# Kernel optimization log

Hardware: AMD Instinct MI355X
Metric: run time of the kernel (lower is better)

Reference implementation:

```python
import jax, jax.numpy as jnp
import numpy as np

N_NODES = 100000
N_EDGES = 3200000
N_PAIRS = 500000
D_IN = 256
D_HID = 256
D_OUT = 2


def setup_inputs() -> dict:
    key = jax.random.key(0)
    ks = jax.random.split(key, 9)
    s1 = 1.0 / np.sqrt(D_IN)
    s2 = 1.0 / np.sqrt(D_HID)
    s3 = 1.0 / np.sqrt(2 * D_HID)
    return {
        "x": jax.random.normal(ks[0], (N_NODES, D_IN), jnp.float32),
        "edge_index": jax.random.randint(ks[1], (2, N_EDGES), 0, N_NODES, jnp.int64 if jax.config.jax_enable_x64 else jnp.int32),
        "index": jax.random.randint(ks[2], (N_PAIRS, 2), 0, N_NODES, jnp.int64 if jax.config.jax_enable_x64 else jnp.int32),
        "W1": jax.random.normal(ks[3], (D_HID, D_IN), jnp.float32) * s1,
        "b1": jnp.zeros((D_HID,), jnp.float32),
        "W2": jax.random.normal(ks[4], (D_HID, D_HID), jnp.float32) * s2,
        "b2": jnp.zeros((D_HID,), jnp.float32),
        "W3": jax.random.normal(ks[5], (D_OUT, 2 * D_HID), jnp.float32) * s3,
        "b3": jnp.zeros((D_OUT,), jnp.float32),
    }


def _gin_conv(x, edge_index, W, b):
    # PyG GINConv (eps=0): nn((1+eps)*x + sum_{j in N(i)} x_j)
    src, dst = edge_index[0], edge_index[1]
    agg = jax.ops.segment_sum(x[src], dst, num_segments=x.shape[0])  # [N, d]
    return (x + agg) @ W.T + b


def reference(x, edge_index, index, W1, b1, W2, b2, W3, b3):
    h = jax.nn.relu(_gin_conv(x, edge_index, W1, b1))   # [N, D_HID]
    h = jax.nn.relu(_gin_conv(h, edge_index, W2, b2))   # [N, D_HID]
    pair = jnp.concatenate((h[index[:, 0]], h[index[:, 1]]), axis=-1)  # [P, 2*D_HID]
    logits = pair @ W3.T + b3                            # [P, D_OUT]
    return jax.nn.log_softmax(logits, axis=1)
```

## Files before the change

### kernel.cpp

```cpp
#include <hip/hip_runtime.h>
#include <hip/hip_bf16.h>

constexpr int N_NODES = 100000;
constexpr int N_EDGES = 3200000;
constexpr int N_PAIRS = 500000;
constexpr int D       = 256;

using frag_ab = __attribute__((ext_vector_type(8))) short;
using frag_cd = __attribute__((ext_vector_type(4))) float;
typedef unsigned short ushort8 __attribute__((ext_vector_type(8)));

static __device__ __forceinline__ float b2f(unsigned short u) {
  return __uint_as_float(((unsigned)u) << 16);
}
static __device__ __forceinline__ unsigned short f2bf(float f) {
  unsigned u = __float_as_uint(f);
  unsigned r = (u + 0x7fff + ((u >> 16) & 1)) >> 16;
  return (unsigned short)r;
}

__global__ void zero_ints(int* __restrict__ p, int n) {
  int i = blockIdx.x * blockDim.x + threadIdx.x;
  if (i < n) p[i] = 0;
}

__global__ void copy_ints(const int* __restrict__ in, int* __restrict__ out, int n) {
  int i = blockIdx.x * blockDim.x + threadIdx.x;
  if (i < n) out[i] = in[i];
}

__global__ void f32_to_bf16(const float4* __restrict__ in, ushort4* __restrict__ out, int n4) {
  int i = blockIdx.x * blockDim.x + threadIdx.x;
  int stride = gridDim.x * blockDim.x;
  for (; i < n4; i += stride) {
    const float4 v = in[i];
    ushort4 o;
    o.x = f2bf(v.x); o.y = f2bf(v.y); o.z = f2bf(v.z); o.w = f2bf(v.w);
    out[i] = o;
  }
}

__global__ void hist_kernel(const int* __restrict__ ei, int* __restrict__ counts) {
  int i = blockIdx.x * blockDim.x + threadIdx.x;
  if (i < N_EDGES) atomicAdd(&counts[ei[N_EDGES + i]], 1);
}

__global__ __launch_bounds__(1024) void scan_kernel(const int* __restrict__ counts,
                                                    int* __restrict__ cursor, int n) {
  __shared__ int wsum[16];
  __shared__ int carry;
  const int t = threadIdx.x, lane = t & 63, w = t >> 6;
  if (t == 0) carry = 0;
  __syncthreads();
  for (int base = 0; base < n; base += 1024) {
    int v = (base + t < n) ? counts[base + t] : 0;
    int s = v;
#pragma unroll
    for (int off = 1; off < 64; off <<= 1) {
      int u = __shfl_up(s, off, 64);
      if (lane >= off) s += u;
    }
    if (lane == 63) wsum[w] = s;
    __syncthreads();
    if (t < 16) {
      int ws = wsum[t];
#pragma unroll
      for (int off = 1; off < 16; off <<= 1) {
        int u = __shfl_up(ws, off, 64);
        if (lane >= off) ws += u;
      }
      wsum[t] = ws;
    }
    __syncthreads();
    const int wpre = (w == 0) ? 0 : wsum[w - 1];
    if (base + t < n) cursor[base + t] = carry + wpre + s - v;
    __syncthreads();
    if (t == 0) carry += wsum[15];
    __syncthreads();
  }
}

constexpr int FILL_SEG = 4096;
__global__ __launch_bounds__(256) void fill_kernel(const int* __restrict__ ei,
                                                   int* __restrict__ pos,
                                                   int* __restrict__ csr) {
  const int range = blockIdx.x & 7;
  const int seg   = blockIdx.x >> 3;
  const int base  = seg * FILL_SEG;
  const int lo = range * 12500, hi = lo + 12500;
#pragma unroll
  for (int j = 0; j < FILL_SEG / 256; ++j) {
    const int i = base + j * 256 + threadIdx.x;
    if (i < N_EDGES) {
      const int dst = ei[N_EDGES + i];
      if (dst >= lo && dst < hi) {
        const int p = atomicAdd(&pos[dst], 1);
        csr[p] = ei[i];
      }
    }
  }
}

__global__ __launch_bounds__(256) void gather_agg_bf16(const ushort* __restrict__ x,
                                                       const int* __restrict__ csr,
                                                       const int* __restrict__ cursor,
                                                       const int* __restrict__ counts,
                                                       ushort* __restrict__ out) {
  const int node = blockIdx.x * 4 + (threadIdx.x >> 6);
  const int lane = threadIdx.x & 63;
  const int half = lane >> 5;
  const int fl   = lane & 31;
  if (node >= N_NODES) return;
  const int beg = cursor[node];
  const int end = beg + counts[node];
  const size_t fo = (size_t)fl * 8;

  float acc[8];
#pragma unroll
  for (int j = 0; j < 8; ++j) acc[j] = 0.f;

  if (half == 0) {
    const ushort8 self = *reinterpret_cast<const ushort8*>(x + (size_t)node * D + fo);
#pragma unroll
    for (int j = 0; j < 8; ++j) acc[j] += b2f(self[j]);
  }

  int o = beg + half;
  for (; o + 6 < end; o += 8) {
    const int s0 = csr[o], s1 = csr[o + 2], s2 = csr[o + 4], s3 = csr[o + 6];
    const ushort8 v0 = *reinterpret_cast<const ushort8*>(x + (size_t)s0 * D + fo);
    const ushort8 v1 = *reinterpret_cast<const ushort8*>(x + (size_t)s1 * D + fo);
    const ushort8 v2 = *reinterpret_cast<const ushort8*>(x + (size_t)s2 * D + fo);
    const ushort8 v3 = *reinterpret_cast<const ushort8*>(x + (size_t)s3 * D + fo);
#pragma unroll
    for (int j = 0; j < 8; ++j)
      acc[j] += (b2f(v0[j]) + b2f(v1[j])) + (b2f(v2[j]) + b2f(v3[j]));
  }
  for (; o < end; o += 2) {
    const ushort8 v = *reinterpret_cast<const ushort8*>(x + (size_t)csr[o] * D + fo);
#pragma unroll
    for (int j = 0; j < 8; ++j) acc[j] += b2f(v[j]);
  }

#pragma unroll
  for (int j = 0; j < 8; ++j) acc[j] += __shfl_xor(acc[j], 32, 64);

  if (half == 0) {
    ushort8 ov;
#pragma unroll
    for (int j = 0; j < 8; ++j) ov[j] = f2bf(acc[j]);
    *reinterpret_cast<ushort8*>(out + (size_t)node * D + fo) = ov;
  }
}

__global__ __launch_bounds__(256) void gemm_mfma_bf16(const ushort* __restrict__ A,
                                                      const ushort* __restrict__ W,
                                                      const float* __restrict__ bias,
                                                      ushort* __restrict__ C,
                                                      int M) {
  __shared__ __align__(16) ushort As[64 * 256];
  __shared__ __align__(16) ushort Ws[64 * 256];

  const int t = threadIdx.x;
  const int w = t >> 6, l = t & 63;
  const int row0 = blockIdx.x * 64;
  const int col0 = blockIdx.y * 64;

  {
    const float4 zero4 = {0.f, 0.f, 0.f, 0.f};
#pragma unroll
    for (int i = 0; i < 8; ++i) {
      const int chunk = t + i * 256;
      const int r  = chunk >> 5;
      const int kb = (chunk & 31) << 4;
      const int swz = kb ^ ((r & 7) << 4);
      const int grow = row0 + r;
      float4 av = zero4;
      if (grow < M)
        av = *reinterpret_cast<const float4*>(
            reinterpret_cast<const char*>(A) + (size_t)grow * 512 + kb);
      *reinterpret_cast<float4*>(reinterpret_cast<char*>(As) + r * 512 + swz) = av;
      const float4 wv = *reinterpret_cast<const float4*>(
          reinterpret_cast<const char*>(W) + (size_t)(col0 + r) * 512 + kb);
      *reinterpret_cast<float4*>(reinterpret_cast<char*>(Ws) + r * 512 + swz) = wv;
    }
  }
  __syncthreads();

  const int g  = l >> 4;
  const int fr = l & 15;

  frag_cd acc[4];
#pragma unroll
  for (int c = 0; c < 4; ++c) {
    acc[c][0] = 0.f; acc[c][1] = 0.f; acc[c][2] = 0.f; acc[c][3] = 0.f;
  }

  const int arow = w * 16 + fr;
  const char* Asb = reinterpret_cast<const char*>(As);
  const char* Wsb = reinterpret_cast<const char*>(Ws);
#pragma unroll
  for (int ks = 0; ks < 8; ++ks) {
    const int kb = ks * 64 + g * 16;
    const frag_ab af = *reinterpret_cast<const frag_ab*>(
        Asb + arow * 512 + (kb ^ ((arow & 7) << 4)));
#pragma unroll
    for (int c = 0; c < 4; ++c) {
      const int wrow = c * 16 + fr;
      const frag_ab bf = *reinterpret_cast<const frag_ab*>(
          Wsb + wrow * 512 + (kb ^ ((wrow & 7) << 4)));
      acc[c] = __builtin_amdgcn_mfma_f32_16x16x32_bf16(af, bf, acc[c], 0, 0, 0);
    }
  }
  __syncthreads();

  ushort* Ct = As;
#pragma unroll
  for (int c = 0; c < 4; ++c) {
    const int col = c * 16 + fr;
    const float bv = bias[col0 + col];
#pragma unroll
    for (int r = 0; r < 4; ++r) {
      const int rl = w * 16 + g * 4 + r;
      Ct[rl * 64 + col] = f2bf(fmaxf(acc[c][r] + bv, 0.f));
    }
  }
  __syncthreads();
#pragma unroll
  for (int i = 0; i < 2; ++i) {
    const int chunk = t + i * 256;
    const int r  = chunk >> 3;
    const int cb = (chunk & 7) << 4;
    const int grow = row0 + r;
    if (grow < M)
      *reinterpret_cast<float4*>(reinterpret_cast<char*>(C) + (size_t)grow * 512 + col0 * 2 + cb) =
          *reinterpret_cast<const float4*>(reinterpret_cast<const char*>(Ct) + r * 128 + cb);
  }
}

__global__ __launch_bounds__(256) void proj_kernel(const ushort* __restrict__ h,
                                                   const float* __restrict__ W3,
                                                   float4* __restrict__ proj) {
  const int node = blockIdx.x * 4 + (threadIdx.x >> 6);
  const int lane = threadIdx.x & 63;
  if (node >= N_NODES) return;

  const ushort4 hv = *reinterpret_cast<const ushort4*>(h + (size_t)node * D + lane * 4);
  const float h0 = b2f(hv.x), h1 = b2f(hv.y), h2 = b2f(hv.z), h3 = b2f(hv.w);

  const float4 wa0 = *reinterpret_cast<const float4*>(W3 + lane * 4);
  const float4 wa1 = *reinterpret_cast<const float4*>(W3 + 512 + lane * 4);
  const float4 wb0 = *reinterpret_cast<const float4*>(W3 + 256 + lane * 4);
  const float4 wb1 = *reinterpret_cast<const float4*>(W3 + 768 + lane * 4);

  float a0 = h0 * wa0.x + h1 * wa0.y + h2 * wa0.z + h3 * wa0.w;
  float a1 = h0 * wa1.x + h1 * wa1.y + h2 * wa1.z + h3 * wa1.w;
  float b0 = h0 * wb0.x + h1 * wb0.y + h2 * wb0.z + h3 * wb0.w;
  float b1 = h0 * wb1.x + h1 * wb1.y + h2 * wb1.z + h3 * wb1.w;

#pragma unroll
  for (int off = 32; off > 0; off >>= 1) {
    a0 += __shfl_xor(a0, off, 64);
    a1 += __shfl_xor(a1, off, 64);
    b0 += __shfl_xor(b0, off, 64);
    b1 += __shfl_xor(b1, off, 64);
  }
  if (lane == 0) {
    float4 o; o.x = a0; o.y = a1; o.z = b0; o.w = b1;
    proj[node] = o;
  }
}

__global__ __launch_bounds__(256) void pair_lite(const float4* __restrict__ proj,
                                                 const int* __restrict__ idx,
                                                 const float* __restrict__ b3,
                                                 float* __restrict__ out) {
  const int p = blockIdx.x * blockDim.x + threadIdx.x;
  if (p >= N_PAIRS) return;
  const int2 ii = reinterpret_cast<const int2*>(idx)[p];
  const float4 pa = proj[ii.x];
  const float4 pb = proj[ii.y];
  float l0 = pa.x + pb.z + b3[0];
  float l1 = pa.y + pb.w + b3[1];
  const float m = fmaxf(l0, l1);
  const float lse = m + logf(expf(l0 - m) + expf(l1 - m));
  float2 o; o.x = l0 - lse; o.y = l1 - lse;
  reinterpret_cast<float2*>(out)[p] = o;
}

extern "C" void kernel_launch(void* const* d_in, const int* in_sizes, int n_in,
                              void* d_out, int out_size, void* d_ws, size_t ws_size,
                              hipStream_t stream) {
  const float* x   = (const float*)d_in[0];
  const int*   ei  = (const int*)d_in[1];
  const int*   idx = (const int*)d_in[2];
  const float* W1  = (const float*)d_in[3];
  const float* b1  = (const float*)d_in[4];
  const float* W2  = (const float*)d_in[5];
  const float* b2  = (const float*)d_in[6];
  const float* W3  = (const float*)d_in[7];
  const float* b3  = (const float*)d_in[8];
  float* out = (float*)d_out;

  char* ws = (char*)d_ws;
  ushort* xb    = (ushort*)(ws);
  ushort* aggb  = (ushort*)(ws + 51200000);
  ushort* hb    = (ushort*)(ws + 102400000);
  ushort* W1b   = (ushort*)(ws + 153600000);
  ushort* W2b   = (ushort*)(ws + 153731072);
  int* counts   = (int*)(ws + 153862144);
  int* cursor   = (int*)(ws + 154262144);
  int* pos      = (int*)(ws + 154662144);
  int* csr      = (int*)(ws + 155062144);
  float4* proj  = (float4*)(ws + 167862144);

  const dim3 blk(256);
  const size_t feat = (size_t)N_NODES * D;
  const dim3 zeroGrid((N_NODES + 255) / 256);
  const dim3 edgeGrid((N_EDGES + 255) / 256);
  const int  nseg = (N_EDGES + FILL_SEG - 1) / FILL_SEG;
  const dim3 fillGrid(8 * nseg);
  const dim3 nodeGrid((N_NODES + 3) / 4);
  const dim3 gemmGrid((N_NODES + 63) / 64, D / 64);
  const dim3 pairGrid((N_PAIRS + 255) / 256);

  f32_to_bf16<<<dim3(4096), blk, 0, stream>>>((const float4*)x, (ushort4*)xb, (int)(feat / 4));
  f32_to_bf16<<<dim3(64), blk, 0, stream>>>((const float4*)W1, (ushort4*)W1b, 65536 / 4);
  f32_to_bf16<<<dim3(64), blk, 0, stream>>>((const float4*)W2, (ushort4*)W2b, 65536 / 4);

  zero_ints<<<zeroGrid, blk, 0, stream>>>(counts, N_NODES);
  hist_kernel<<<edgeGrid, blk, 0, stream>>>(ei, counts);
  scan_kernel<<<1, 1024, 0, stream>>>(counts, cursor, N_NODES);
  copy_ints<<<zeroGrid, blk, 0, stream>>>(cursor, pos, N_NODES);
  fill_kernel<<<fillGrid, blk, 0, stream>>>(ei, pos, csr);

  gather_agg_bf16<<<nodeGrid, blk, 0, stream>>>(xb, csr, cursor, counts, aggb);
  gemm_mfma_bf16<<<gemmGrid, blk, 0, stream>>>(aggb, W1b, b1, hb, N_NODES);

  gather_agg_bf16<<<nodeGrid, blk, 0, stream>>>(hb, csr, cursor, counts, aggb);
  gemm_mfma_bf16<<<gemmGrid, blk, 0, stream>>>(aggb, W2b, b2, hb, N_NODES);

  proj_kernel<<<nodeGrid, blk, 0, stream>>>(hb, W3, proj);
  pair_lite<<<pairGrid, blk, 0, stream>>>(proj, idx, b3, out);
}
```

Measured before the change: 990.8 us.

## Parallelize CSR build with multi-block scan and range-bucketed edge partition

```diff
diff --git a/kernel.cpp b/kernel.cpp
--- a/kernel.cpp
+++ b/kernel.cpp
@@ -5,6 +5,9 @@
 constexpr int N_EDGES = 3200000;
 constexpr int N_PAIRS = 500000;
 constexpr int D       = 256;
+constexpr int NRANGE  = 8;
+constexpr int RSPAN   = 12500;
+constexpr int SCANN   = 100352;
 
 using frag_ab = __attribute__((ext_vector_type(8))) short;
 using frag_cd = __attribute__((ext_vector_type(4))) float;
@@ -22,11 +25,6 @@
 __global__ void zero_ints(int* __restrict__ p, int n) {
   int i = blockIdx.x * blockDim.x + threadIdx.x;
   if (i < n) p[i] = 0;
-}
-
-__global__ void copy_ints(const int* __restrict__ in, int* __restrict__ out, int n) {
-  int i = blockIdx.x * blockDim.x + threadIdx.x;
-  if (i < n) out[i] = in[i];
 }
 
 __global__ void f32_to_bf16(const float4* __restrict__ in, ushort4* __restrict__ out, int n4) {
@@ -40,64 +38,139 @@
   }
 }
 
+__global__ void conv_weights(const float4* __restrict__ W1, const float4* __restrict__ W2,
+                             ushort4* __restrict__ W1b, ushort4* __restrict__ W2b) {
+  const int i = blockIdx.x * blockDim.x + threadIdx.x;
+  const bool second = i >= 16384;
+  const int k = second ? i - 16384 : i;
+  if (k < 16384) {
+    const float4 v = second ? W2[k] : W1[k];
+    ushort4 o;
+    o.x = f2bf(v.x); o.y = f2bf(v.y); o.z = f2bf(v.z); o.w = f2bf(v.w);
+    if (second) W2b[k] = o; else W1b[k] = o;
+  }
+}
+
 __global__ void hist_kernel(const int* __restrict__ ei, int* __restrict__ counts) {
   int i = blockIdx.x * blockDim.x + threadIdx.x;
   if (i < N_EDGES) atomicAdd(&counts[ei[N_EDGES + i]], 1);
 }
 
-__global__ __launch_bounds__(1024) void scan_kernel(const int* __restrict__ counts,
-                                                    int* __restrict__ cursor, int n) {
+__global__ __launch_bounds__(1024) void scan_block_k(const int* __restrict__ in,
+                                                     int* __restrict__ out,
+                                                     int* __restrict__ bsum) {
   __shared__ int wsum[16];
-  __shared__ int carry;
   const int t = threadIdx.x, lane = t & 63, w = t >> 6;
-  if (t == 0) carry = 0;
-  __syncthreads();
-  for (int base = 0; base < n; base += 1024) {
-    int v = (base + t < n) ? counts[base + t] : 0;
-    int s = v;
-#pragma unroll
-    for (int off = 1; off < 64; off <<= 1) {
-      int u = __shfl_up(s, off, 64);
-      if (lane >= off) s += u;
-    }
-    if (lane == 63) wsum[w] = s;
-    __syncthreads();
-    if (t < 16) {
-      int ws = wsum[t];
-#pragma unroll
-      for (int off = 1; off < 16; off <<= 1) {
-        int u = __shfl_up(ws, off, 64);
-        if (lane >= off) ws += u;
-      }
-      wsum[t] = ws;
-    }
-    __syncthreads();
-    const int wpre = (w == 0) ? 0 : wsum[w - 1];
-    if (base + t < n) cursor[base + t] = carry + wpre + s - v;
-    __syncthreads();
-    if (t == 0) carry += wsum[15];
-    __syncthreads();
-  }
-}
-
-constexpr int FILL_SEG = 4096;
-__global__ __launch_bounds__(256) void fill_kernel(const int* __restrict__ ei,
+  const int gid = blockIdx.x * 1024 + t;
+  const int v = in[gid];
+  int s = v;
+#pragma unroll
+  for (int off = 1; off < 64; off <<= 1) {
+    int u = __shfl_up(s, off, 64);
+    if (lane >= off) s += u;
+  }
+  if (lane == 63) wsum[w] = s;
+  __syncthreads();
+  if (t < 16) {
+    int ws = wsum[t];
+#pragma unroll
+    for (int off = 1; off < 16; off <<= 1) {
+      int u = __shfl_up(ws, off, 64);
+      if (lane >= off) ws += u;
+    }
+    wsum[t] = ws;
+  }
+  __syncthreads();
+  const int wpre = (w == 0) ? 0 : wsum[w - 1];
+  out[gid] = wpre + s - v;
+  if (t == 1023) bsum[blockIdx.x] = wsum[15];
+}
+
+__global__ __launch_bounds__(1024) void scan_small(const int* __restrict__ in,
+                                                   int* __restrict__ out, int n) {
+  __shared__ int wsum[16];
+  const int t = threadIdx.x, lane = t & 63, w = t >> 6;
+  int v = (t < n) ? in[t] : 0;
+  int s = v;
+#pragma unroll
+  for (int off = 1; off < 64; off <<= 1) {
+    int u = __shfl_up(s, off, 64);
+    if (lane >= off) s += u;
+  }
+  if (lane == 63) wsum[w] = s;
+  __syncthreads();
+  if (t < 16) {
+    int ws = wsum[t];
+#pragma unroll
+    for (int off = 1; off < 16; off <<= 1) {
+      int u = __shfl_up(ws, off, 64);
+      if (lane >= off) ws += u;
+    }
+    wsum[t] = ws;
+  }
+  __syncthreads();
+  const int wpre = (w == 0) ? 0 : wsum[w - 1];
+  if (t < n) out[t] = wpre + s - v;
+}
+
+__global__ __launch_bounds__(1024) void scan_add_k(int* __restrict__ cursor,
                                                    int* __restrict__ pos,
-                                                   int* __restrict__ csr) {
-  const int range = blockIdx.x & 7;
-  const int seg   = blockIdx.x >> 3;
-  const int base  = seg * FILL_SEG;
-  const int lo = range * 12500, hi = lo + 12500;
-#pragma unroll
-  for (int j = 0; j < FILL_SEG / 256; ++j) {
-    const int i = base + j * 256 + threadIdx.x;
+                                                   const int* __restrict__ bsum2,
+                                                   int* __restrict__ rc) {
+  const int gid = blockIdx.x * 1024 + threadIdx.x;
+  const int v = cursor[gid] + bsum2[gid >> 10];
+  cursor[gid] = v;
+  pos[gid] = v;
+  if (gid < N_NODES && gid % RSPAN == 0) rc[gid / RSPAN] = v;
+}
+
+constexpr int PART_SEG = 4096;
+__global__ __launch_bounds__(256) void partition_kernel(const int* __restrict__ ei,
+                                                        int* __restrict__ rc,
+                                                        int2* __restrict__ bucket) {
+  __shared__ int lcnt[NRANGE];
+  __shared__ int lbase[NRANGE];
+  const int t = threadIdx.x;
+  const int base = blockIdx.x * PART_SEG;
+  if (t < NRANGE) lcnt[t] = 0;
+  __syncthreads();
+
+  int rnk[16], rng[16], sv[16], dv[16];
+#pragma unroll
+  for (int j = 0; j < 16; ++j) {
+    const int i = base + j * 256 + t;
     if (i < N_EDGES) {
-      const int dst = ei[N_EDGES + i];
-      if (dst >= lo && dst < hi) {
-        const int p = atomicAdd(&pos[dst], 1);
-        csr[p] = ei[i];
-      }
-    }
+      sv[j] = ei[i];
+      dv[j] = ei[N_EDGES + i];
+      rng[j] = dv[j] / RSPAN;
+      rnk[j] = atomicAdd(&lcnt[rng[j]], 1);
+    } else rng[j] = -1;
+  }
+  __syncthreads();
+  if (t < NRANGE) lbase[t] = atomicAdd(&rc[t], lcnt[t]);
+  __syncthreads();
+#pragma unroll
+  for (int j = 0; j < 16; ++j) {
+    if (rng[j] >= 0) {
+      int2 e; e.x = sv[j]; e.y = dv[j];
+      bucket[lbase[rng[j]] + rnk[j]] = e;
+    }
+  }
+}
+
+constexpr int FLB = 128;
+__global__ __launch_bounds__(256) void fill_local(const int2* __restrict__ bucket,
+                                                  const int* __restrict__ cursor,
+                                                  int* __restrict__ pos,
+                                                  int* __restrict__ csr) {
+  const int r = blockIdx.x & 7;
+  const int j = blockIdx.x >> 3;
+  const int beg = cursor[(size_t)r * RSPAN];
+  const int end = (r < 7) ? cursor[(size_t)(r + 1) * RSPAN] : N_EDGES;
+  for (int i = beg + j * 256 + threadIdx.x; i < end; i += FLB * 256) {
+    const int2 e = bucket[i];
+    const int p = atomicAdd(&pos[e.y], 1);
+    csr[p] = e.x;
   }
 }
 
@@ -305,34 +378,40 @@
   char* ws = (char*)d_ws;
   ushort* xb    = (ushort*)(ws);
   ushort* aggb  = (ushort*)(ws + 51200000);
+  int2*   bucket= (int2*)(ws + 51200000);
   ushort* hb    = (ushort*)(ws + 102400000);
   ushort* W1b   = (ushort*)(ws + 153600000);
   ushort* W2b   = (ushort*)(ws + 153731072);
   int* counts   = (int*)(ws + 153862144);
-  int* cursor   = (int*)(ws + 154262144);
-  int* pos      = (int*)(ws + 154662144);
-  int* csr      = (int*)(ws + 155062144);
-  float4* proj  = (float4*)(ws + 167862144);
+  int* cursor   = (int*)(ws + 154263552);
+  int* pos      = (int*)(ws + 154664960);
+  int* csr      = (int*)(ws + 155066368);
+  float4* proj  = (float4*)(ws + 167866368);
+  int* bsum     = (int*)(ws + 169466368);
+  int* bsum2    = (int*)(ws + 169466880);
+  int* rc       = (int*)(ws + 169467392);
 
   const dim3 blk(256);
   const size_t feat = (size_t)N_NODES * D;
-  const dim3 zeroGrid((N_NODES + 255) / 256);
+  constexpr int SCAN_BLOCKS = SCANN / 1024;
   const dim3 edgeGrid((N_EDGES + 255) / 256);
-  const int  nseg = (N_EDGES + FILL_SEG - 1) / FILL_SEG;
-  const dim3 fillGrid(8 * nseg);
+  const dim3 partGrid((N_EDGES + PART_SEG - 1) / PART_SEG);
+  const dim3 flocGrid(NRANGE * FLB);
   const dim3 nodeGrid((N_NODES + 3) / 4);
   const dim3 gemmGrid((N_NODES + 63) / 64, D / 64);
   const dim3 pairGrid((N_PAIRS + 255) / 256);
 
   f32_to_bf16<<<dim3(4096), blk, 0, stream>>>((const float4*)x, (ushort4*)xb, (int)(feat / 4));
-  f32_to_bf16<<<dim3(64), blk, 0, stream>>>((const float4*)W1, (ushort4*)W1b, 65536 / 4);
-  f32_to_bf16<<<dim3(64), blk, 0, stream>>>((const float4*)W2, (ushort4*)W2b, 65536 / 4);
-
-  zero_ints<<<zeroGrid, blk, 0, stream>>>(counts, N_NODES);
+  conv_weights<<<dim3(128), blk, 0, stream>>>((const float4*)W1, (const float4*)W2,
+                                              (ushort4*)W1b, (ushort4*)W2b);
+
+  zero_ints<<<dim3((SCANN + 255) / 256), blk, 0, stream>>>(counts, SCANN);
   hist_kernel<<<edgeGrid, blk, 0, stream>>>(ei, counts);
-  scan_kernel<<<1, 1024, 0, stream>>>(counts, cursor, N_NODES);
-  copy_ints<<<zeroGrid, blk, 0, stream>>>(cursor, pos, N_NODES);
-  fill_kernel<<<fillGrid, blk, 0, stream>>>(ei, pos, csr);
+  scan_block_k<<<dim3(SCAN_BLOCKS), dim3(1024), 0, stream>>>(counts, cursor, bsum);
+  scan_small<<<1, 1024, 0, stream>>>(bsum, bsum2, SCAN_BLOCKS);
+  scan_add_k<<<dim3(SCAN_BLOCKS), dim3(1024), 0, stream>>>(cursor, pos, bsum2, rc);
+  partition_kernel<<<partGrid, blk, 0, stream>>>(ei, rc, bucket);
+  fill_local<<<flocGrid, blk, 0, stream>>>(bucket, cursor, pos, csr);
 
   gather_agg_bf16<<<nodeGrid, blk, 0, stream>>>(xb, csr, cursor, counts, aggb);
   gemm_mfma_bf16<<<gemmGrid, blk, 0, stream>>>(aggb, W1b, b1, hb, N_NODES);
```

After: 915.9 us. 7.6% less time.
